# Optimization experiments

Hardware: AMD Instinct MI355X
Metric: run time of the kernel (lower is better)

The kernel has to match this reference:

```python
import jax, jax.numpy as jnp
import numpy as np

B, L1, L2, D = 32, 512, 512, 1024


def setup_inputs() -> dict:
    key = jax.random.key(0)
    k1, k2, k3, k4 = jax.random.split(key, 4)
    v1 = jax.random.normal(k1, (B, L1, D), dtype=jnp.float32)
    v2 = jax.random.normal(k2, (B, L2, D), dtype=jnp.float32)
    # row/column is fully masked (which would NaN the softmax).
    v1_mask = jax.random.uniform(k3, (B, L1)) < 0.2
    v2_mask = jax.random.uniform(k4, (B, L2)) < 0.2
    return {"v1": v1, "v2": v2, "v1_mask": v1_mask, "v2_mask": v2_mask}


def reference(v1, v2, v1_mask, v2_mask):
    # similarity: [B, L1, L2]
    sim = jnp.einsum("bid,bjd->bij", v1, v2)
    neg_inf = jnp.float32(-jnp.inf)
    # softmax over v2 positions (dim=2), masking padded v2 columns
    v1_v2_attn = jax.nn.softmax(
        jnp.where(v2_mask[:, None, :], neg_inf, sim), axis=2)
    # softmax over v1 positions (dim=1), masking padded v1 rows
    v2_v1_attn = jax.nn.softmax(
        jnp.where(v1_mask[:, :, None], neg_inf, sim), axis=1)
    attended_v1 = jnp.einsum("bij,bjd->bid", v1_v2_attn, v2)  # [B,L1,D]
    attended_v2 = jnp.einsum("bij,bid->bjd", v2_v1_attn, v1)  # [B,L2,D]
    attended_v1 = jnp.where(v1_mask[:, :, None], 0.0, attended_v1)
    attended_v2 = jnp.where(v2_mask[:, :, None], 0.0, attended_v2)
    return attended_v1, attended_v2
```

## Files before the change

### kernel.cpp

```cpp
#include <hip/hip_runtime.h>
#include <stdint.h>


#define Bn 32
#define Ln 512
#define Dn 1024

typedef __attribute__((ext_vector_type(4))) float f32x4;
typedef __attribute__((ext_vector_type(4))) unsigned short u16x4;
typedef __attribute__((ext_vector_type(8))) unsigned short u16x8;
typedef __attribute__((ext_vector_type(8))) __bf16 bf16x8;

union bfcast { u16x8 u; bf16x8 b; };

__device__ __forceinline__ unsigned short f2bf(float f) {
  unsigned int u = __float_as_uint(f);
  u += 0x7FFFu + ((u >> 16) & 1u);
  return (unsigned short)(u >> 16);
}

__device__ __forceinline__ void async_cp16(const void* g, void* l) {
  __builtin_amdgcn_global_load_lds(
      (__attribute__((address_space(1))) void*)(g),
      (__attribute__((address_space(3))) void*)(l), 16, 0, 0);
}

__device__ __forceinline__ void cvt8(f32x4 x0, f32x4 x1,
                                     bf16x8* hi, bf16x8* lo) {
  float xs[8] = {x0[0], x0[1], x0[2], x0[3], x1[0], x1[1], x1[2], x1[3]};
  u16x8 h, l;
#pragma unroll
  for (int e = 0; e < 8; e++) {
    unsigned int u = __float_as_uint(xs[e]);
    h[e] = (unsigned short)(u >> 16);
    float hf = __uint_as_float(u & 0xFFFF0000u);
    l[e] = (unsigned short)(__float_as_uint(xs[e] - hf) >> 16);
  }
  bfcast ch, cl;
  ch.u = h; cl.u = l;
  *hi = ch.b; *lo = cl.b;
}

__global__ __launch_bounds__(256) void conv_t(
    const float* __restrict__ v1, const float* __restrict__ v2,
    unsigned short* __restrict__ v1t, unsigned short* __restrict__ v2t) {
  __shared__ float tile[64][65];
  const int z = blockIdx.z;
  const float* src = (z < Bn) ? v1 : v2;
  unsigned short* dt = (z < Bn) ? v1t : v2t;
  const int b = z & 31;
  const int d0 = blockIdx.x << 6;
  const int l0 = blockIdx.y << 6;
  const int tid = threadIdx.x;
#pragma unroll
  for (int it = 0; it < 4; it++) {
    int lin = (it << 8) + tid;
    int l = lin >> 4;
    int d4 = (lin & 15) << 2;
    f32x4 x = *(const f32x4*)(src + (size_t)(b * Ln + l0 + l) * Dn + d0 + d4);
    tile[l][d4] = x[0]; tile[l][d4 + 1] = x[1];
    tile[l][d4 + 2] = x[2]; tile[l][d4 + 3] = x[3];
  }
  __syncthreads();
#pragma unroll
  for (int it = 0; it < 4; it++) {
    int lin = (it << 8) + tid;
    int d = lin >> 4;
    int l4 = (lin & 15) << 2;
    u16x4 o;
    o[0] = f2bf(tile[l4][d]);     o[1] = f2bf(tile[l4 + 1][d]);
    o[2] = f2bf(tile[l4 + 2][d]); o[3] = f2bf(tile[l4 + 3][d]);
    *(u16x4*)(dt + (size_t)(b * Dn + d0 + d) * Ln + l0 + l4) = o;
  }
}

__global__ __launch_bounds__(256) void sim_gemm_split(
    const float* __restrict__ V1, const float* __restrict__ V2,
    float* __restrict__ C) {
  __shared__ float As[128 * 32];
  __shared__ float Bs[128 * 32];
  const int b = blockIdx.z;
  const float* Ab = V1 + (size_t)b * Ln * Dn;
  const float* Bb = V2 + (size_t)b * Ln * Dn;
  float* Cb = C + (size_t)b * Ln * Ln;
  const int m0 = blockIdx.y << 7;
  const int n0 = blockIdx.x << 7;
  const int tid = threadIdx.x;
  const int lane = tid & 63;
  const int wave = tid >> 6;
  const int wrow = (wave >> 1) << 6;
  const int wcol = (wave & 1) << 6;

  const int srow = lane >> 3;
  const int scol = ((lane & 7) ^ srow) << 2;
  const float* ga = Ab + (size_t)(m0 + (wave << 5) + srow) * Dn + scol;
  const float* gb = Bb + (size_t)(n0 + (wave << 5) + srow) * Dn + scol;

  const int r = lane & 15;
  const int q = lane >> 4;

  const f32x4 zero4 = {0.f, 0.f, 0.f, 0.f};
  f32x4 acc[4][4];
#pragma unroll
  for (int i = 0; i < 4; i++)
#pragma unroll
    for (int j = 0; j < 4; j++) acc[i][j] = zero4;

  for (int k0 = 0; k0 < Dn; k0 += 32) {
    __syncthreads();
#pragma unroll
    for (int j = 0; j < 4; j++) {
      async_cp16(ga + k0 + j * 8 * Dn, As + ((wave << 5) + j * 8) * 32);
      async_cp16(gb + k0 + j * 8 * Dn, Bs + ((wave << 5) + j * 8) * 32);
    }
    __syncthreads();
    bf16x8 ah[4], al[4], bh[4], bl[4];
#pragma unroll
    for (int t = 0; t < 4; t++) {
      int ra = wrow + (t << 4) + r;
      f32x4 x0 = *(const f32x4*)(As + ra * 32 + ((((q << 1)    ) ^ (ra & 7)) << 2));
      f32x4 x1 = *(const f32x4*)(As + ra * 32 + ((((q << 1) | 1) ^ (ra & 7)) << 2));
      cvt8(x0, x1, &ah[t], &al[t]);
      int rb = wcol + (t << 4) + r;
      f32x4 y0 = *(const f32x4*)(Bs + rb * 32 + ((((q << 1)    ) ^ (rb & 7)) << 2));
      f32x4 y1 = *(const f32x4*)(Bs + rb * 32 + ((((q << 1) | 1) ^ (rb & 7)) << 2));
      cvt8(y0, y1, &bh[t], &bl[t]);
    }
#pragma unroll
    for (int tm = 0; tm < 4; tm++)
#pragma unroll
      for (int tn = 0; tn < 4; tn++) {
        acc[tm][tn] = __builtin_amdgcn_mfma_f32_16x16x32_bf16(
            ah[tm], bh[tn], acc[tm][tn], 0, 0, 0);
        acc[tm][tn] = __builtin_amdgcn_mfma_f32_16x16x32_bf16(
            ah[tm], bl[tn], acc[tm][tn], 0, 0, 0);
        acc[tm][tn] = __builtin_amdgcn_mfma_f32_16x16x32_bf16(
            al[tm], bh[tn], acc[tm][tn], 0, 0, 0);
      }
  }

#pragma unroll
  for (int tm = 0; tm < 4; tm++) {
    int rowb = m0 + wrow + (tm << 4) + (q << 2);
#pragma unroll
    for (int reg = 0; reg < 4; reg++) {
      int row = rowb + reg;
#pragma unroll
      for (int tn = 0; tn < 4; tn++) {
        int col = n0 + wcol + (tn << 4) + r;
        Cb[(size_t)row * Ln + col] = acc[tm][tn][reg];
      }
    }
  }
}

__global__ __launch_bounds__(256) void gemm_nt(
    const unsigned short* __restrict__ A, const unsigned short* __restrict__ Bm,
    float* __restrict__ C, const int* __restrict__ rowmask,
    int M, int N, int K) {
  __shared__ unsigned short As[128 * 32];
  __shared__ unsigned short Bs[128 * 32];
  const int b = blockIdx.z;
  const unsigned short* Ab = A + (size_t)b * M * K;
  const unsigned short* Bb = Bm + (size_t)b * N * K;
  float* Cb = C + (size_t)b * M * N;
  const int m0 = blockIdx.y << 7;
  const int n0 = blockIdx.x << 7;
  const int tid = threadIdx.x;
  const int lane = tid & 63;
  const int wave = tid >> 6;
  const int wrow = (wave >> 1) << 6;
  const int wcol = (wave & 1) << 6;

  const int srow = tid >> 2;
  const int skof = (tid & 3) << 3;
  const unsigned short* ga0 = Ab + (size_t)(m0 + srow) * K + skof;
  const unsigned short* ga1 = Ab + (size_t)(m0 + 64 + srow) * K + skof;
  const unsigned short* gb0 = Bb + (size_t)(n0 + srow) * K + skof;
  const unsigned short* gb1 = Bb + (size_t)(n0 + 64 + srow) * K + skof;

  const int r = lane & 15;
  const int q = lane >> 4;

  const f32x4 zero4 = {0.f, 0.f, 0.f, 0.f};
  f32x4 acc[4][4];
#pragma unroll
  for (int i = 0; i < 4; i++)
#pragma unroll
    for (int j = 0; j < 4; j++) acc[i][j] = zero4;

  for (int k0 = 0; k0 < K; k0 += 32) {
    __syncthreads();
    async_cp16(ga0 + k0, As + (wave << 9));
    async_cp16(ga1 + k0, As + 2048 + (wave << 9));
    async_cp16(gb0 + k0, Bs + (wave << 9));
    async_cp16(gb1 + k0, Bs + 2048 + (wave << 9));
    __syncthreads();
    bf16x8 af[4], bf[4];
#pragma unroll
    for (int t = 0; t < 4; t++) {
      af[t] = *(const bf16x8*)(As + ((wrow + (t << 4) + r) << 5) + (q << 3));
      bf[t] = *(const bf16x8*)(Bs + ((wcol + (t << 4) + r) << 5) + (q << 3));
    }
#pragma unroll
    for (int tm = 0; tm < 4; tm++)
#pragma unroll
      for (int tn = 0; tn < 4; tn++)
        acc[tm][tn] = __builtin_amdgcn_mfma_f32_16x16x32_bf16(
            af[tm], bf[tn], acc[tm][tn], 0, 0, 0);
  }

  const int* mb = rowmask ? rowmask + b * M : (const int*)0;
#pragma unroll
  for (int tm = 0; tm < 4; tm++) {
    int rowb = m0 + wrow + (tm << 4) + (q << 2);
#pragma unroll
    for (int reg = 0; reg < 4; reg++) {
      int row = rowb + reg;
      float mz = (mb && mb[row]) ? 0.f : 1.f;
#pragma unroll
      for (int tn = 0; tn < 4; tn++) {
        int col = n0 + wcol + (tn << 4) + r;
        Cb[(size_t)row * N + col] = acc[tm][tn][reg] * mz;
      }
    }
  }
}

__global__ __launch_bounds__(256) void row_softmax(
    const float* __restrict__ sim, const int* __restrict__ v2m,
    unsigned short* __restrict__ A1) {
  const int row = (blockIdx.x << 2) + (threadIdx.x >> 6);
  const int lane = threadIdx.x & 63;
  const int b = row >> 9;
  const float* s = sim + (size_t)row * Ln;
  const int* mk = v2m + (b << 9);
  const float NEGINF = -__builtin_inff();
  float v[8];
  float mx = NEGINF;
#pragma unroll
  for (int t = 0; t < 8; t++) {
    int j = lane + (t << 6);
    float x = mk[j] ? NEGINF : s[j];
    v[t] = x;
    mx = fmaxf(mx, x);
  }
#pragma unroll
  for (int off = 32; off > 0; off >>= 1) mx = fmaxf(mx, __shfl_xor(mx, off));
  float sum = 0.f;
#pragma unroll
  for (int t = 0; t < 8; t++) {
    float e = (v[t] > NEGINF) ? __expf(v[t] - mx) : 0.f;
    v[t] = e;
    sum += e;
  }
#pragma unroll
  for (int off = 32; off > 0; off >>= 1) sum += __shfl_xor(sum, off);
  float rs = 1.f / sum;
  unsigned short* o = A1 + (size_t)row * Ln;
#pragma unroll
  for (int t = 0; t < 8; t++) o[lane + (t << 6)] = f2bf(v[t] * rs);
}

__global__ __launch_bounds__(256) void csm_part(
    const float* __restrict__ sim, const int* __restrict__ v1m,
    float* __restrict__ pmax, float* __restrict__ psum) {
  __shared__ float sm[4][64], ss[4][64];
  const int b = blockIdx.z;
  const int ic = blockIdx.y;
  const int i0 = ic << 6;
  const int j0 = blockIdx.x << 6;
  const int tx = threadIdx.x & 63;
  const int ty = threadIdx.x >> 6;
  const float* S = sim + (size_t)b * (Ln * Ln) + j0 + tx;
  const int* mk = v1m + (b << 9) + i0;
  const float NEGINF = -__builtin_inff();
  float x[16];
#pragma unroll
  for (int k = 0; k < 16; k++) {
    int il = (k << 2) + ty;
    float v = S[(size_t)(i0 + il) * Ln];
    x[k] = mk[il] ? NEGINF : v;
  }
  float m = NEGINF;
#pragma unroll
  for (int k = 0; k < 16; k++) m = fmaxf(m, x[k]);
  float s = 0.f;
#pragma unroll
  for (int k = 0; k < 16; k++) s += (x[k] > NEGINF) ? __expf(x[k] - m) : 0.f;
  sm[ty][tx] = m;
  ss[ty][tx] = s;
  __syncthreads();
  if (ty == 0) {
    float M = fmaxf(fmaxf(sm[0][tx], sm[1][tx]), fmaxf(sm[2][tx], sm[3][tx]));
    float Sv = 0.f;
#pragma unroll
    for (int p = 0; p < 4; p++)
      Sv += (sm[p][tx] > NEGINF) ? ss[p][tx] * __expf(sm[p][tx] - M) : 0.f;
    int idx = (((b << 3) + ic) << 9) + j0 + tx;
    pmax[idx] = M;
    psum[idx] = Sv;
  }
}

__global__ __launch_bounds__(256) void csm_comb(
    const float* __restrict__ pmax, const float* __restrict__ psum,
    float* __restrict__ cmax, float* __restrict__ crs) {
  const int col = (blockIdx.x << 8) + threadIdx.x;
  const int b = col >> 9;
  const int j = col & 511;
  const float NEGINF = -__builtin_inff();
  float mm[8], sv[8];
#pragma unroll
  for (int p = 0; p < 8; p++) {
    int idx = (((b << 3) + p) << 9) + j;
    mm[p] = pmax[idx];
    sv[p] = psum[idx];
  }
  float M = NEGINF;
#pragma unroll
  for (int p = 0; p < 8; p++) M = fmaxf(M, mm[p]);
  float Sv = 0.f;
#pragma unroll
  for (int p = 0; p < 8; p++)
    Sv += (mm[p] > NEGINF) ? sv[p] * __expf(mm[p] - M) : 0.f;
  cmax[col] = M;
  crs[col] = 1.f / Sv;
}

__global__ __launch_bounds__(256) void csm_write(
    const float* __restrict__ sim, const int* __restrict__ v1m,
    const float* __restrict__ cmax, const float* __restrict__ crs,
    unsigned short* __restrict__ A2t) {
  __shared__ float cm[64], cr[64];
  __shared__ unsigned short Tc[64][66];
  const int b = blockIdx.z;
  const int i0 = blockIdx.y << 6;
  const int j0 = blockIdx.x << 6;
  const int tx = threadIdx.x & 63;
  const int ty = threadIdx.x >> 6;
  if (threadIdx.x < 64) {
    cm[threadIdx.x] = cmax[(b << 9) + j0 + threadIdx.x];
    cr[threadIdx.x] = crs[(b << 9) + j0 + threadIdx.x];
  }
  __syncthreads();
  const float* S = sim + (size_t)b * (Ln * Ln) + j0 + tx;
  const int* mk = v1m + (b << 9) + i0;
  const float cmx = cm[tx];
  const float cs = cr[tx];
#pragma unroll
  for (int k = 0; k < 16; k++) {
    int il = (k << 2) + ty;
    float x = S[(size_t)(i0 + il) * Ln];
    float e = mk[il] ? 0.f : __expf(x - cmx) * cs;
    Tc[tx][il] = f2bf(e);
  }
  __syncthreads();
  unsigned short* o = A2t + ((size_t)(b << 9) + j0) * Ln + i0;
#pragma unroll
  for (int t = 0; t < 4; t++) {
    int c = (t << 8) + (int)threadIdx.x;
    int j = c >> 4;
    int ch = c & 15;
    u16x4 v;
    v[0] = Tc[j][(ch << 2)];     v[1] = Tc[j][(ch << 2) + 1];
    v[2] = Tc[j][(ch << 2) + 2]; v[3] = Tc[j][(ch << 2) + 3];
    *(u16x4*)(o + (size_t)j * Ln + (ch << 2)) = v;
  }
}

extern "C" void kernel_launch(void* const* d_in, const int* in_sizes, int n_in,
                              void* d_out, int out_size, void* d_ws,
                              size_t ws_size, hipStream_t stream) {
  (void)in_sizes; (void)n_in; (void)out_size; (void)ws_size;
  const float* v1 = (const float*)d_in[0];
  const float* v2 = (const float*)d_in[1];
  const int* v1m = (const int*)d_in[2];
  const int* v2m = (const int*)d_in[3];
  float* out1 = (float*)d_out;
  float* out2 = out1 + (size_t)Bn * Ln * Dn;

  char* ws = (char*)d_ws;
  const size_t Mi = 1048576;
  unsigned short* v1t = (unsigned short*)(ws);
  unsigned short* v2t = (unsigned short*)(ws + 32 * Mi);
  float* sim = (float*)(ws + 64 * Mi);
  unsigned short* A1 = (unsigned short*)(ws + 96 * Mi);
  unsigned short* A2t = (unsigned short*)(ws + 112 * Mi);
  float* pmax = (float*)(ws + 128 * Mi);
  float* psum = (float*)(ws + 128 * Mi + 512 * 1024);
  float* cmax = (float*)(ws + 129 * Mi);
  float* crs = (float*)(ws + 129 * Mi + 64 * 1024);

  dim3 blk(256);
  conv_t<<<dim3(16, 8, 64), blk, 0, stream>>>(v1, v2, v1t, v2t);
  sim_gemm_split<<<dim3(4, 4, 32), blk, 0, stream>>>(v1, v2, sim);
  row_softmax<<<dim3(4096), blk, 0, stream>>>(sim, v2m, A1);
  csm_part<<<dim3(8, 8, 32), blk, 0, stream>>>(sim, v1m, pmax, psum);
  csm_comb<<<dim3(64), blk, 0, stream>>>(pmax, psum, cmax, crs);
  csm_write<<<dim3(8, 8, 32), blk, 0, stream>>>(sim, v1m, cmax, crs, A2t);
  gemm_nt<<<dim3(8, 4, 32), blk, 0, stream>>>(A1, v2t, out1, v1m,
                                              512, 1024, 512);
  gemm_nt<<<dim3(8, 4, 32), blk, 0, stream>>>(A2t, v1t, out2, v2m,
                                              512, 1024, 512);
}
```

Before: 424.6 us.

## Precompute bf16 hi/lo splits in conversion pass, use fp16 for value GEMMs

The conversion kernel now also writes bf16 high and low halves of v1 and v2 in row-major layout. The similarity GEMM then loads these precomputed halves directly instead of splitting fp32 tiles in registers on every k-step, which removes the repeated per-tile conversion ALU work. The attention and value operands move from bf16 to fp16 for better mantissa precision in the output GEMMs. The column-softmax combine kernel is folded into csm_write. In exchange the conversion pass writes 64 MB of extra hi/lo data and the sim GEMM stages four bf16 tiles per step instead of two fp32 tiles.

```diff
diff --git a/kernel.cpp b/kernel.cpp
--- a/kernel.cpp
+++ b/kernel.cpp
@@ -8,16 +8,9 @@
 
 typedef __attribute__((ext_vector_type(4))) float f32x4;
 typedef __attribute__((ext_vector_type(4))) unsigned short u16x4;
-typedef __attribute__((ext_vector_type(8))) unsigned short u16x8;
 typedef __attribute__((ext_vector_type(8))) __bf16 bf16x8;
-
-union bfcast { u16x8 u; bf16x8 b; };
-
-__device__ __forceinline__ unsigned short f2bf(float f) {
-  unsigned int u = __float_as_uint(f);
-  u += 0x7FFFu + ((u >> 16) & 1u);
-  return (unsigned short)(u >> 16);
-}
+typedef __attribute__((ext_vector_type(8))) _Float16 f16x8;
+typedef __attribute__((ext_vector_type(4))) _Float16 f16x4;
 
 __device__ __forceinline__ void async_cp16(const void* g, void* l) {
   __builtin_amdgcn_global_load_lds(
@@ -25,29 +18,17 @@
       (__attribute__((address_space(3))) void*)(l), 16, 0, 0);
 }
 
-__device__ __forceinline__ void cvt8(f32x4 x0, f32x4 x1,
-                                     bf16x8* hi, bf16x8* lo) {
-  float xs[8] = {x0[0], x0[1], x0[2], x0[3], x1[0], x1[1], x1[2], x1[3]};
-  u16x8 h, l;
-#pragma unroll
-  for (int e = 0; e < 8; e++) {
-    unsigned int u = __float_as_uint(xs[e]);
-    h[e] = (unsigned short)(u >> 16);
-    float hf = __uint_as_float(u & 0xFFFF0000u);
-    l[e] = (unsigned short)(__float_as_uint(xs[e] - hf) >> 16);
-  }
-  bfcast ch, cl;
-  ch.u = h; cl.u = l;
-  *hi = ch.b; *lo = cl.b;
-}
-
-__global__ __launch_bounds__(256) void conv_t(
+__global__ __launch_bounds__(256) void conv_split_t(
     const float* __restrict__ v1, const float* __restrict__ v2,
-    unsigned short* __restrict__ v1t, unsigned short* __restrict__ v2t) {
+    unsigned short* __restrict__ v1h, unsigned short* __restrict__ v1l,
+    unsigned short* __restrict__ v2h, unsigned short* __restrict__ v2l,
+    _Float16* __restrict__ v1t, _Float16* __restrict__ v2t) {
   __shared__ float tile[64][65];
   const int z = blockIdx.z;
   const float* src = (z < Bn) ? v1 : v2;
-  unsigned short* dt = (z < Bn) ? v1t : v2t;
+  unsigned short* dh = (z < Bn) ? v1h : v2h;
+  unsigned short* dl = (z < Bn) ? v1l : v2l;
+  _Float16* dt = (z < Bn) ? v1t : v2t;
   const int b = z & 31;
   const int d0 = blockIdx.x << 6;
   const int l0 = blockIdx.y << 6;
@@ -57,7 +38,18 @@
     int lin = (it << 8) + tid;
     int l = lin >> 4;
     int d4 = (lin & 15) << 2;
-    f32x4 x = *(const f32x4*)(src + (size_t)(b * Ln + l0 + l) * Dn + d0 + d4);
+    size_t base = (size_t)(b * Ln + l0 + l) * Dn + d0 + d4;
+    f32x4 x = *(const f32x4*)(src + base);
+    u16x4 h, lo;
+#pragma unroll
+    for (int e = 0; e < 4; e++) {
+      unsigned int u = __float_as_uint(x[e]);
+      h[e] = (unsigned short)(u >> 16);
+      float hf = __uint_as_float(u & 0xFFFF0000u);
+      lo[e] = (unsigned short)(__float_as_uint(x[e] - hf) >> 16);
+    }
+    *(u16x4*)(dh + base) = h;
+    *(u16x4*)(dl + base) = lo;
     tile[l][d4] = x[0]; tile[l][d4 + 1] = x[1];
     tile[l][d4 + 2] = x[2]; tile[l][d4 + 3] = x[3];
   }
@@ -67,21 +59,20 @@
     int lin = (it << 8) + tid;
     int d = lin >> 4;
     int l4 = (lin & 15) << 2;
-    u16x4 o;
-    o[0] = f2bf(tile[l4][d]);     o[1] = f2bf(tile[l4 + 1][d]);
-    o[2] = f2bf(tile[l4 + 2][d]); o[3] = f2bf(tile[l4 + 3][d]);
-    *(u16x4*)(dt + (size_t)(b * Dn + d0 + d) * Ln + l0 + l4) = o;
-  }
-}
-
-__global__ __launch_bounds__(256) void sim_gemm_split(
-    const float* __restrict__ V1, const float* __restrict__ V2,
+    f16x4 o;
+    o[0] = (_Float16)tile[l4][d];     o[1] = (_Float16)tile[l4 + 1][d];
+    o[2] = (_Float16)tile[l4 + 2][d]; o[3] = (_Float16)tile[l4 + 3][d];
+    *(f16x4*)(dt + (size_t)(b * Dn + d0 + d) * Ln + l0 + l4) = o;
+  }
+}
+
+__global__ __launch_bounds__(256) void sim_gemm3(
+    const unsigned short* __restrict__ Ah_, const unsigned short* __restrict__ Al_,
+    const unsigned short* __restrict__ Bh_, const unsigned short* __restrict__ Bl_,
     float* __restrict__ C) {
-  __shared__ float As[128 * 32];
-  __shared__ float Bs[128 * 32];
+  __shared__ unsigned short AsH[4096], AsL[4096], BsH[4096], BsL[4096];
   const int b = blockIdx.z;
-  const float* Ab = V1 + (size_t)b * Ln * Dn;
-  const float* Bb = V2 + (size_t)b * Ln * Dn;
+  const size_t boff = (size_t)b * Ln * Dn;
   float* Cb = C + (size_t)b * Ln * Ln;
   const int m0 = blockIdx.y << 7;
   const int n0 = blockIdx.x << 7;
@@ -91,10 +82,16 @@
   const int wrow = (wave >> 1) << 6;
   const int wcol = (wave & 1) << 6;
 
-  const int srow = lane >> 3;
-  const int scol = ((lane & 7) ^ srow) << 2;
-  const float* ga = Ab + (size_t)(m0 + (wave << 5) + srow) * Dn + scol;
-  const float* gb = Bb + (size_t)(n0 + (wave << 5) + srow) * Dn + scol;
+  const int srow = tid >> 2;
+  const int skof = (tid & 3) << 3;
+  const unsigned short* gah0 = Ah_ + boff + (size_t)(m0 + srow) * Dn + skof;
+  const unsigned short* gah1 = gah0 + (size_t)64 * Dn;
+  const unsigned short* gal0 = Al_ + boff + (size_t)(m0 + srow) * Dn + skof;
+  const unsigned short* gal1 = gal0 + (size_t)64 * Dn;
+  const unsigned short* gbh0 = Bh_ + boff + (size_t)(n0 + srow) * Dn + skof;
+  const unsigned short* gbh1 = gbh0 + (size_t)64 * Dn;
+  const unsigned short* gbl0 = Bl_ + boff + (size_t)(n0 + srow) * Dn + skof;
+  const unsigned short* gbl1 = gbl0 + (size_t)64 * Dn;
 
   const int r = lane & 15;
   const int q = lane >> 4;
@@ -108,23 +105,24 @@
 
   for (int k0 = 0; k0 < Dn; k0 += 32) {
     __syncthreads();
-#pragma unroll
-    for (int j = 0; j < 4; j++) {
-      async_cp16(ga + k0 + j * 8 * Dn, As + ((wave << 5) + j * 8) * 32);
-      async_cp16(gb + k0 + j * 8 * Dn, Bs + ((wave << 5) + j * 8) * 32);
-    }
+    async_cp16(gah0 + k0, AsH + (wave << 9));
+    async_cp16(gah1 + k0, AsH + 2048 + (wave << 9));
+    async_cp16(gal0 + k0, AsL + (wave << 9));
+    async_cp16(gal1 + k0, AsL + 2048 + (wave << 9));
+    async_cp16(gbh0 + k0, BsH + (wave << 9));
+    async_cp16(gbh1 + k0, BsH + 2048 + (wave << 9));
+    async_cp16(gbl0 + k0, BsL + (wave << 9));
+    async_cp16(gbl1 + k0, BsL + 2048 + (wave << 9));
     __syncthreads();
     bf16x8 ah[4], al[4], bh[4], bl[4];
 #pragma unroll
     for (int t = 0; t < 4; t++) {
-      int ra = wrow + (t << 4) + r;
-      f32x4 x0 = *(const f32x4*)(As + ra * 32 + ((((q << 1)    ) ^ (ra & 7)) << 2));
-      f32x4 x1 = *(const f32x4*)(As + ra * 32 + ((((q << 1) | 1) ^ (ra & 7)) << 2));
-      cvt8(x0, x1, &ah[t], &al[t]);
-      int rb = wcol + (t << 4) + r;
-      f32x4 y0 = *(const f32x4*)(Bs + rb * 32 + ((((q << 1)    ) ^ (rb & 7)) << 2));
-      f32x4 y1 = *(const f32x4*)(Bs + rb * 32 + ((((q << 1) | 1) ^ (rb & 7)) << 2));
-      cvt8(y0, y1, &bh[t], &bl[t]);
+      int oa = ((wrow + (t << 4) + r) << 5) + (q << 3);
+      int ob = ((wcol + (t << 4) + r) << 5) + (q << 3);
+      ah[t] = *(const bf16x8*)(AsH + oa);
+      al[t] = *(const bf16x8*)(AsL + oa);
+      bh[t] = *(const bf16x8*)(BsH + ob);
+      bl[t] = *(const bf16x8*)(BsL + ob);
     }
 #pragma unroll
     for (int tm = 0; tm < 4; tm++)
@@ -154,15 +152,15 @@
   }
 }
 
-__global__ __launch_bounds__(256) void gemm_nt(
-    const unsigned short* __restrict__ A, const unsigned short* __restrict__ Bm,
+__global__ __launch_bounds__(256) void gemm_nt_f16(
+    const _Float16* __restrict__ A, const _Float16* __restrict__ Bm,
     float* __restrict__ C, const int* __restrict__ rowmask,
     int M, int N, int K) {
-  __shared__ unsigned short As[128 * 32];
-  __shared__ unsigned short Bs[128 * 32];
+  __shared__ _Float16 As[128 * 32];
+  __shared__ _Float16 Bs[128 * 32];
   const int b = blockIdx.z;
-  const unsigned short* Ab = A + (size_t)b * M * K;
-  const unsigned short* Bb = Bm + (size_t)b * N * K;
+  const _Float16* Ab = A + (size_t)b * M * K;
+  const _Float16* Bb = Bm + (size_t)b * N * K;
   float* Cb = C + (size_t)b * M * N;
   const int m0 = blockIdx.y << 7;
   const int n0 = blockIdx.x << 7;
@@ -174,10 +172,10 @@
 
   const int srow = tid >> 2;
   const int skof = (tid & 3) << 3;
-  const unsigned short* ga0 = Ab + (size_t)(m0 + srow) * K + skof;
-  const unsigned short* ga1 = Ab + (size_t)(m0 + 64 + srow) * K + skof;
-  const unsigned short* gb0 = Bb + (size_t)(n0 + srow) * K + skof;
-  const unsigned short* gb1 = Bb + (size_t)(n0 + 64 + srow) * K + skof;
+  const _Float16* ga0 = Ab + (size_t)(m0 + srow) * K + skof;
+  const _Float16* ga1 = Ab + (size_t)(m0 + 64 + srow) * K + skof;
+  const _Float16* gb0 = Bb + (size_t)(n0 + srow) * K + skof;
+  const _Float16* gb1 = Bb + (size_t)(n0 + 64 + srow) * K + skof;
 
   const int r = lane & 15;
   const int q = lane >> 4;
@@ -196,17 +194,17 @@
     async_cp16(gb0 + k0, Bs + (wave << 9));
     async_cp16(gb1 + k0, Bs + 2048 + (wave << 9));
     __syncthreads();
-    bf16x8 af[4], bf[4];
+    f16x8 af[4], bf[4];
 #pragma unroll
     for (int t = 0; t < 4; t++) {
-      af[t] = *(const bf16x8*)(As + ((wrow + (t << 4) + r) << 5) + (q << 3));
-      bf[t] = *(const bf16x8*)(Bs + ((wcol + (t << 4) + r) << 5) + (q << 3));
+      af[t] = *(const f16x8*)(As + ((wrow + (t << 4) + r) << 5) + (q << 3));
+      bf[t] = *(const f16x8*)(Bs + ((wcol + (t << 4) + r) << 5) + (q << 3));
     }
 #pragma unroll
     for (int tm = 0; tm < 4; tm++)
 #pragma unroll
       for (int tn = 0; tn < 4; tn++)
-        acc[tm][tn] = __builtin_amdgcn_mfma_f32_16x16x32_bf16(
+        acc[tm][tn] = __builtin_amdgcn_mfma_f32_16x16x32_f16(
             af[tm], bf[tn], acc[tm][tn], 0, 0, 0);
   }
 
@@ -229,7 +227,7 @@
 
 __global__ __launch_bounds__(256) void row_softmax(
     const float* __restrict__ sim, const int* __restrict__ v2m,
-    unsigned short* __restrict__ A1) {
+    _Float16* __restrict__ A1) {
   const int row = (blockIdx.x << 2) + (threadIdx.x >> 6);
   const int lane = threadIdx.x & 63;
   const int b = row >> 9;
@@ -257,9 +255,9 @@
 #pragma unroll
   for (int off = 32; off > 0; off >>= 1) sum += __shfl_xor(sum, off);
   float rs = 1.f / sum;
-  unsigned short* o = A1 + (size_t)row * Ln;
-#pragma unroll
-  for (int t = 0; t < 8; t++) o[lane + (t << 6)] = f2bf(v[t] * rs);
+  _Float16* o = A1 + (size_t)row * Ln;
+#pragma unroll
+  for (int t = 0; t < 8; t++) o[lane + (t << 6)] = (_Float16)(v[t] * rs);
 }
 
 __global__ __launch_bounds__(256) void csm_part(
@@ -303,45 +301,35 @@
   }
 }
 
-__global__ __launch_bounds__(256) void csm_comb(
-    const float* __restrict__ pmax, const float* __restrict__ psum,
-    float* __restrict__ cmax, float* __restrict__ crs) {
-  const int col = (blockIdx.x << 8) + threadIdx.x;
-  const int b = col >> 9;
-  const int j = col & 511;
-  const float NEGINF = -__builtin_inff();
-  float mm[8], sv[8];
-#pragma unroll
-  for (int p = 0; p < 8; p++) {
-    int idx = (((b << 3) + p) << 9) + j;
-    mm[p] = pmax[idx];
-    sv[p] = psum[idx];
-  }
-  float M = NEGINF;
-#pragma unroll
-  for (int p = 0; p < 8; p++) M = fmaxf(M, mm[p]);
-  float Sv = 0.f;
-#pragma unroll
-  for (int p = 0; p < 8; p++)
-    Sv += (mm[p] > NEGINF) ? sv[p] * __expf(mm[p] - M) : 0.f;
-  cmax[col] = M;
-  crs[col] = 1.f / Sv;
-}
-
 __global__ __launch_bounds__(256) void csm_write(
     const float* __restrict__ sim, const int* __restrict__ v1m,
-    const float* __restrict__ cmax, const float* __restrict__ crs,
-    unsigned short* __restrict__ A2t) {
+    const float* __restrict__ pmax, const float* __restrict__ psum,
+    _Float16* __restrict__ A2t) {
   __shared__ float cm[64], cr[64];
-  __shared__ unsigned short Tc[64][66];
+  __shared__ _Float16 Tc[64][66];
   const int b = blockIdx.z;
   const int i0 = blockIdx.y << 6;
   const int j0 = blockIdx.x << 6;
   const int tx = threadIdx.x & 63;
   const int ty = threadIdx.x >> 6;
+  const float NEGINF = -__builtin_inff();
   if (threadIdx.x < 64) {
-    cm[threadIdx.x] = cmax[(b << 9) + j0 + threadIdx.x];
-    cr[threadIdx.x] = crs[(b << 9) + j0 + threadIdx.x];
+    int j = j0 + (int)threadIdx.x;
+    float M = NEGINF;
+    float mm[8], sv[8];
+#pragma unroll
+    for (int p = 0; p < 8; p++) {
+      int idx = (((b << 3) + p) << 9) + j;
+      mm[p] = pmax[idx];
+      sv[p] = psum[idx];
+      M = fmaxf(M, mm[p]);
+    }
+    float Sv = 0.f;
+#pragma unroll
+    for (int p = 0; p < 8; p++)
+      Sv += (mm[p] > NEGINF) ? sv[p] * __expf(mm[p] - M) : 0.f;
+    cm[threadIdx.x] = M;
+    cr[threadIdx.x] = 1.f / Sv;
   }
   __syncthreads();
   const float* S = sim + (size_t)b * (Ln * Ln) + j0 + tx;
@@ -353,19 +341,19 @@
     int il = (k << 2) + ty;
     float x = S[(size_t)(i0 + il) * Ln];
     float e = mk[il] ? 0.f : __expf(x - cmx) * cs;
-    Tc[tx][il] = f2bf(e);
+    Tc[tx][il] = (_Float16)e;
   }
   __syncthreads();
-  unsigned short* o = A2t + ((size_t)(b << 9) + j0) * Ln + i0;
+  _Float16* o = A2t + ((size_t)(b << 9) + j0) * Ln + i0;
 #pragma unroll
   for (int t = 0; t < 4; t++) {
     int c = (t << 8) + (int)threadIdx.x;
     int j = c >> 4;
     int ch = c & 15;
-    u16x4 v;
+    f16x4 v;
     v[0] = Tc[j][(ch << 2)];     v[1] = Tc[j][(ch << 2) + 1];
     v[2] = Tc[j][(ch << 2) + 2]; v[3] = Tc[j][(ch << 2) + 3];
-    *(u16x4*)(o + (size_t)j * Ln + (ch << 2)) = v;
+    *(f16x4*)(o + (size_t)j * Ln + (ch << 2)) = v;
   }
 }
 
@@ -382,25 +370,27 @@
 
   char* ws = (char*)d_ws;
   const size_t Mi = 1048576;
-  unsigned short* v1t = (unsigned short*)(ws);
-  unsigned short* v2t = (unsigned short*)(ws + 32 * Mi);
-  float* sim = (float*)(ws + 64 * Mi);
-  unsigned short* A1 = (unsigned short*)(ws + 96 * Mi);
-  unsigned short* A2t = (unsigned short*)(ws + 112 * Mi);
-  float* pmax = (float*)(ws + 128 * Mi);
-  float* psum = (float*)(ws + 128 * Mi + 512 * 1024);
-  float* cmax = (float*)(ws + 129 * Mi);
-  float* crs = (float*)(ws + 129 * Mi + 64 * 1024);
+  unsigned short* v1h = (unsigned short*)(ws);
+  unsigned short* v1l = (unsigned short*)(ws + 32 * Mi);
+  unsigned short* v2h = (unsigned short*)(ws + 64 * Mi);
+  unsigned short* v2l = (unsigned short*)(ws + 96 * Mi);
+  _Float16* v1t = (_Float16*)(ws + 128 * Mi);
+  _Float16* v2t = (_Float16*)(ws + 160 * Mi);
+  float* sim = (float*)(ws + 192 * Mi);
+  _Float16* A1 = (_Float16*)(ws + 224 * Mi);
+  _Float16* A2t = (_Float16*)(ws + 240 * Mi);
+  float* pmax = (float*)(ws + 256 * Mi);
+  float* psum = (float*)(ws + 256 * Mi + 512 * 1024);
 
   dim3 blk(256);
-  conv_t<<<dim3(16, 8, 64), blk, 0, stream>>>(v1, v2, v1t, v2t);
-  sim_gemm_split<<<dim3(4, 4, 32), blk, 0, stream>>>(v1, v2, sim);
+  conv_split_t<<<dim3(16, 8, 64), blk, 0, stream>>>(v1, v2, v1h, v1l, v2h,
+                                                    v2l, v1t, v2t);
+  sim_gemm3<<<dim3(4, 4, 32), blk, 0, stream>>>(v1h, v1l, v2h, v2l, sim);
   row_softmax<<<dim3(4096), blk, 0, stream>>>(sim, v2m, A1);
   csm_part<<<dim3(8, 8, 32), blk, 0, stream>>>(sim, v1m, pmax, psum);
-  csm_comb<<<dim3(64), blk, 0, stream>>>(pmax, psum, cmax, crs);
-  csm_write<<<dim3(8, 8, 32), blk, 0, stream>>>(sim, v1m, cmax, crs, A2t);
-  gemm_nt<<<dim3(8, 4, 32), blk, 0, stream>>>(A1, v2t, out1, v1m,
-                                              512, 1024, 512);
-  gemm_nt<<<dim3(8, 4, 32), blk, 0, stream>>>(A2t, v1t, out2, v2m,
-                                              512, 1024, 512);
-}
+  csm_write<<<dim3(8, 8, 32), blk, 0, stream>>>(sim, v1m, pmax, psum, A2t);
+  gemm_nt_f16<<<dim3(8, 4, 32), blk, 0, stream>>>(A1, v2t, out1, v1m,
+                                                  512, 1024, 512);
+  gemm_nt_f16<<<dim3(8, 4, 32), blk, 0, stream>>>(A2t, v1t, out2, v2m,
+                                                  512, 1024, 512);
+}
```

New measurement: 452.6 us. 6.6% more time.
